# Kernel optimization log

Measured on AMD Instinct MI355X. Metric: run time of the kernel, lower is better.

## Reference

```python
import jax, jax.numpy as jnp
import numpy as np

HIDDEN = 128
N_RBF = 20
K = 16
CUTOFF = 5.0


def setup_inputs() -> dict:
    key = jax.random.key(0)
    ks = jax.random.split(key, 12)
    B, N, D = 8, 4096, HIDDEN
    edge_in = 2 * D + N_RBF  # 276
    s = 0.02
    return {
        "h": jax.random.normal(ks[0], (B, N, D), jnp.float32),
        "positions": jax.random.normal(ks[1], (B, N, 3), jnp.float32),
        # edge MLP: Linear(276->128), SiLU, Linear(128->128), SiLU
        "ew1": jax.random.normal(ks[2], (edge_in, D), jnp.float32) * s,
        "eb1": jnp.zeros((D,), jnp.float32),
        "ew2": jax.random.normal(ks[3], (D, D), jnp.float32) * s,
        "eb2": jnp.zeros((D,), jnp.float32),
        # node MLP: Linear(256->128), SiLU, (Dropout=identity in eval), Linear(128->128)
        "nw1": jax.random.normal(ks[4], (2 * D, D), jnp.float32) * s,
        "nb1": jnp.zeros((D,), jnp.float32),
        "nw2": jax.random.normal(ks[5], (D, D), jnp.float32) * s,
        "nb2": jnp.zeros((D,), jnp.float32),
        # LayerNorm
        "gamma": jnp.ones((D,), jnp.float32),
        "beta": jnp.zeros((D,), jnp.float32),
    }


def reference(h, positions, ew1, eb1, ew2, eb2, nw1, nb1, nw2, nb2, gamma, beta):
    B, N, D = h.shape
    k = min(K, N - 1)

    # ---- kNN graph build (dense pairwise, self masked with +inf) ----
    diff = positions[:, :, None, :] - positions[:, None, :, :]      # [B,N,N,3]
    dists = jnp.sqrt(jnp.sum(diff * diff, axis=-1) + 1e-8)          # [B,N,N]
    eye = jnp.eye(N, dtype=bool)
    dists_masked = jnp.where(eye[None], jnp.inf, dists)
    _, edge_idx = jax.lax.top_k(-dists_masked, k)                   # [B,N,k] smallest dists
    edge_dist = jnp.take_along_axis(dists_masked, edge_idx, axis=-1)  # [B,N,k]
    edge_mask = edge_dist < CUTOFF                                  # [B,N,k]

    # ---- RBF distance encoding (non-trainable buffers) ----
    centers = jnp.linspace(0.0, CUTOFF, N_RBF)                      # [n_rbf]
    widths = (CUTOFF / N_RBF) ** (-2)
    rbf = jnp.exp(-widths * (edge_dist[..., None] - centers) ** 2)  # [B,N,k,n_rbf]

    # ---- gather neighbor features ----
    h_j = jax.vmap(lambda hb, ib: hb[ib])(h, edge_idx)              # [B,N,k,D]
    h_i = jnp.broadcast_to(h[:, :, None, :], h_j.shape)             # [B,N,k,D]
    edge_features = jnp.concatenate([h_i, h_j, rbf], axis=-1)       # [B,N,k,2D+n_rbf]

    # ---- edge MLP + mask + scatter-sum aggregate ----
    m = jax.nn.silu(edge_features @ ew1 + eb1)
    m = jax.nn.silu(m @ ew2 + eb2)
    m = m * edge_mask[..., None].astype(m.dtype)
    agg = jnp.sum(m, axis=2)                                        # [B,N,D]

    # ---- node MLP (dropout is identity at eval) + residual + LayerNorm ----
    node_in = jnp.concatenate([h, agg], axis=-1)                    # [B,N,2D]
    update = jax.nn.silu(node_in @ nw1 + nb1) @ nw2 + nb2
    x = h + update
    mu = jnp.mean(x, axis=-1, keepdims=True)
    var = jnp.mean((x - mu) ** 2, axis=-1, keepdims=True)
    return (x - mu) / jnp.sqrt(var + 1e-5) * gamma + beta
```

## Files before the change

### kernel.cpp

```cpp
#include <hip/hip_runtime.h>

#define HID 128
#define NRBF 20
#define KNN 16
#define NNODE 4096
#define NBATCH 8
#define CAP 112

typedef __attribute__((ext_vector_type(8))) short short8;
typedef __attribute__((ext_vector_type(4))) float f32x4;

__device__ __forceinline__ short f2bf(float x) {
  unsigned u = __builtin_bit_cast(unsigned, x);
  u = u + 0x7FFFu + ((u >> 16) & 1u);
  return (short)(u >> 16);
}
__device__ __forceinline__ float silu_f(float x) {
  return x * __builtin_amdgcn_rcpf(1.0f + __expf(-x));
}
__device__ __forceinline__ short8 cv8(const float* p) {
  f32x4 a = *(const f32x4*)p;
  f32x4 b = *(const f32x4*)(p + 4);
  short8 r;
  r[0]=f2bf(a[0]); r[1]=f2bf(a[1]); r[2]=f2bf(a[2]); r[3]=f2bf(a[3]);
  r[4]=f2bf(b[0]); r[5]=f2bf(b[1]); r[6]=f2bf(b[2]); r[7]=f2bf(b[3]);
  return r;
}

__global__ __launch_bounds__(256)
void hcvt_kernel(const float* __restrict__ h, short* __restrict__ hb)
{
  size_t i = ((size_t)blockIdx.x * 256 + threadIdx.x) * 8;
  *(short8*)(hb + i) = cv8(h + i);
}

__global__ __launch_bounds__(512)
void knn_kernel(const float* __restrict__ pos,
                int* __restrict__ eidx, float* __restrict__ edist)
{
  __shared__ float pX[NNODE], pY[NNODE], pZ[NNODE];
  __shared__ float d2b[8][4][CAP];
  __shared__ int   jb[8][4][CAP];
  __shared__ int   cntL[8][4];

  const int tid  = threadIdx.x;
  const int wv   = tid >> 6;
  const int lane = tid & 63;
  const int b    = blockIdx.x >> 7;
  const int grp  = blockIdx.x & 127;

  const float* pb = pos + (size_t)b * NNODE * 3;
  for (int idx = tid; idx < NNODE; idx += 512) {
    pX[idx] = pb[idx*3]; pY[idx] = pb[idx*3+1]; pZ[idx] = pb[idx*3+2];
  }
  __syncthreads();

  const int i0 = grp * 32 + wv * 4;
  float pix[4], piy[4], piz[4];
  #pragma unroll
  for (int n = 0; n < 4; ++n) { pix[n]=pX[i0+n]; piy[n]=pY[i0+n]; piz[n]=pZ[i0+n]; }

  float vmin[4] = {3.0e38f, 3.0e38f, 3.0e38f, 3.0e38f};
  #pragma unroll 4
  for (int t = 0; t < 64; ++t) {
    const int j = t * 64 + lane;
    const float x = pX[j], y = pY[j], z = pZ[j];
    #pragma unroll
    for (int n = 0; n < 4; ++n) {
      float dx = __fsub_rn(pix[n], x);
      float dy = __fsub_rn(piy[n], y);
      float dz = __fsub_rn(piz[n], z);
      float d2 = __fadd_rn(__fadd_rn(__fmul_rn(dx,dx), __fmul_rn(dy,dy)), __fmul_rn(dz,dz));
      vmin[n] = fminf(vmin[n], d2);
    }
  }

  float Ts[4];
  #pragma unroll
  for (int n = 0; n < 4; ++n) {
    float v = vmin[n];
    #pragma unroll
    for (int k = 2; k <= 64; k <<= 1) {
      #pragma unroll
      for (int jj = k >> 1; jj > 0; jj >>= 1) {
        float o = __shfl_xor(v, jj);
        const bool up   = ((lane & k) == 0);
        const bool lowl = ((lane & jj) == 0);
        float mn = fminf(v, o), mx = fmaxf(v, o);
        v = (up == lowl) ? mn : mx;
      }
    }
    Ts[n] = __shfl(v, 16);
  }

  if (lane < 4) cntL[wv][lane] = 0;
  #pragma unroll 2
  for (int t = 0; t < 64; ++t) {
    const int j = t * 64 + lane;
    const float x = pX[j], y = pY[j], z = pZ[j];
    #pragma unroll
    for (int n = 0; n < 4; ++n) {
      float dx = __fsub_rn(pix[n], x);
      float dy = __fsub_rn(piy[n], y);
      float dz = __fsub_rn(piz[n], z);
      float d2 = __fadd_rn(__fadd_rn(__fmul_rn(dx,dx), __fmul_rn(dy,dy)), __fmul_rn(dz,dz));
      if ((j != i0 + n) && (d2 <= Ts[n])) {
        int p = atomicAdd(&cntL[wv][n], 1);
        if (p < CAP) { d2b[wv][n][p] = d2; jb[wv][n][p] = j; }
      }
    }
  }

  #pragma unroll 1
  for (int n = 0; n < 4; ++n) {
    int cnt = cntL[wv][n];
    if (cnt > CAP) cnt = CAP;
    for (int s = lane; s < cnt; s += 64) {
      float dm = d2b[wv][n][s]; int jm = jb[wv][n][s];
      int rank = 0;
      for (int c = 0; c < cnt; ++c) {
        float dc = d2b[wv][n][c]; int jc = jb[wv][n][c];
        if (dc < dm || (dc == dm && jc < jm)) ++rank;
      }
      if (rank < KNN) {
        size_t base = ((size_t)b * NNODE + i0 + n) * KNN;
        eidx[base + rank]  = b * NNODE + jm;
        edist[base + rank] = sqrtf(__fadd_rn(dm, 1e-8f));
      }
    }
  }
}

#define ENPW 16

template<bool HBF>
__global__ __launch_bounds__(512)
void edge_kernel(const float* __restrict__ h, const short* __restrict__ hb,
                 const int* __restrict__ eidx, const float* __restrict__ edist,
                 const float* __restrict__ ew1, const float* __restrict__ eb1,
                 const float* __restrict__ ew2, const float* __restrict__ eb2,
                 float* __restrict__ agg)
{
  __shared__ __attribute__((aligned(16))) short8 F1[9*8*64];
  __shared__ __attribute__((aligned(16))) short8 F2[4*8*64];
  __shared__ __attribute__((aligned(16))) short m1s[8][2048];

  const int tid = threadIdx.x;
  for (int f = tid; f < 9*8*64; f += 512) {
    int kc = f >> 9, rem = f & 511, nf = rem >> 6, ln = rem & 63;
    int kb = kc*32 + (ln >> 4)*8, col = nf*16 + (ln & 15);
    short8 v;
    #pragma unroll
    for (int e = 0; e < 8; ++e) {
      int k = kb + e;
      v[e] = (k < 276) ? f2bf(ew1[k*128 + col]) : (short)0;
    }
    F1[f] = v;
  }
  for (int f = tid; f < 4*8*64; f += 512) {
    int kc = f >> 9, rem = f & 511, nf = rem >> 6, ln = rem & 63;
    int kb = kc*32 + (ln >> 4)*8, col = nf*16 + (ln & 15);
    short8 v;
    #pragma unroll
    for (int e = 0; e < 8; ++e) v[e] = f2bf(ew2[(kb + e)*128 + col]);
    F2[f] = v;
  }
  __syncthreads();

  const int wv = tid >> 6, lane = tid & 63;
  const int lo = lane & 15, hi = lane >> 4;
  short* m1w = &m1s[wv][0];

  float b1v[8], b2v[8];
  #pragma unroll
  for (int nf = 0; nf < 8; ++nf) {
    b1v[nf] = eb1[nf*16 + lo];
    b2v[nf] = eb2[nf*16 + lo];
  }
  int wbase[4], xmask[4], rbase[4];
  #pragma unroll
  for (int q = 0; q < 4; ++q) {
    int row = hi*4 + q;
    wbase[q] = (row << 8) + (lo << 1);
    xmask[q] = (row & 7) << 4;
  }
  #pragma unroll
  for (int kc = 0; kc < 4; ++kc)
    rbase[kc] = ((lo << 8) + ((kc*32 + hi*8) << 1)) ^ ((lo & 7) << 4);

  const f32x4 zero4 = {0.f, 0.f, 0.f, 0.f};
  const int nbase = (blockIdx.x * 8 + wv) * ENPW;

  #pragma unroll 1
  for (int it = 0; it < ENPW/2; ++it) {
    const int nA = nbase + it*2, nB = nA + 1;
    int jgA = eidx[(size_t)nA*KNN + lo] & (NBATCH*NNODE - 1);
    int jgB = eidx[(size_t)nB*KNN + lo] & (NBATCH*NNODE - 1);
    const float deA = edist[(size_t)nA*KNN + lo];
    const float deB = edist[(size_t)nB*KNN + lo];

    short8 aIA[4], aJA[4], aIB[4], aJB[4];
    #pragma unroll
    for (int kc = 0; kc < 4; ++kc) {
      if constexpr (HBF) {
        aIA[kc] = *(const short8*)(hb + (size_t)nA*HID  + kc*32 + hi*8);
        aJA[kc] = *(const short8*)(hb + (size_t)jgA*HID + kc*32 + hi*8);
        aIB[kc] = *(const short8*)(hb + (size_t)nB*HID  + kc*32 + hi*8);
        aJB[kc] = *(const short8*)(hb + (size_t)jgB*HID + kc*32 + hi*8);
      } else {
        aIA[kc] = cv8(h + (size_t)nA*HID  + kc*32 + hi*8);
        aJA[kc] = cv8(h + (size_t)jgA*HID + kc*32 + hi*8);
        aIB[kc] = cv8(h + (size_t)nB*HID  + kc*32 + hi*8);
        aJB[kc] = cv8(h + (size_t)jgB*HID + kc*32 + hi*8);
      }
    }
    short8 aRA, aRB;
    #pragma unroll
    for (int e = 0; e < 8; ++e) {
      const int r = hi*8 + e;
      float vA = 0.f, vB = 0.f;
      if (r < NRBF) {
        const float cr = (float)(r * (5.0/19.0));
        float tA = __fsub_rn(deA, cr), tB = __fsub_rn(deB, cr);
        vA = __expf(-16.0f * __fmul_rn(tA, tA));
        vB = __expf(-16.0f * __fmul_rn(tB, tB));
      }
      aRA[e] = f2bf(vA); aRB[e] = f2bf(vB);
    }

    f32x4 acc1A[8], acc1B[8];
    #pragma unroll
    for (int nf = 0; nf < 8; ++nf) { acc1A[nf] = zero4; acc1B[nf] = zero4; }
    __builtin_amdgcn_s_setprio(1);
    #pragma unroll
    for (int kc = 0; kc < 9; ++kc) {
      short8 aA = (kc < 4) ? aIA[kc] : ((kc < 8) ? aJA[kc-4] : aRA);
      short8 aB = (kc < 4) ? aIB[kc] : ((kc < 8) ? aJB[kc-4] : aRB);
      #pragma unroll
      for (int nf = 0; nf < 8; ++nf) {
        short8 bf = F1[(kc*8 + nf)*64 + lane];
        acc1A[nf] = __builtin_amdgcn_mfma_f32_16x16x32_bf16(aA, bf, acc1A[nf], 0,0,0);
        acc1B[nf] = __builtin_amdgcn_mfma_f32_16x16x32_bf16(aB, bf, acc1B[nf], 0,0,0);
      }
    }
    __builtin_amdgcn_s_setprio(0);

    short8 a2A[4], a2B[4];
    #pragma unroll
    for (int nf = 0; nf < 8; ++nf) {
      #pragma unroll
      for (int q = 0; q < 4; ++q) {
        int off = (wbase[q] + (nf << 5)) ^ xmask[q];
        *(short*)((char*)m1w + off) = f2bf(silu_f(acc1A[nf][q] + b1v[nf]));
      }
    }
    #pragma unroll
    for (int kc = 0; kc < 4; ++kc)
      a2A[kc] = *(const short8*)((char*)m1w + rbase[kc]);
    #pragma unroll
    for (int nf = 0; nf < 8; ++nf) {
      #pragma unroll
      for (int q = 0; q < 4; ++q) {
        int off = (wbase[q] + (nf << 5)) ^ xmask[q];
        *(short*)((char*)m1w + off) = f2bf(silu_f(acc1B[nf][q] + b1v[nf]));
      }
    }
    #pragma unroll
    for (int kc = 0; kc < 4; ++kc)
      a2B[kc] = *(const short8*)((char*)m1w + rbase[kc]);

    f32x4 acc2A[8], acc2B[8];
    #pragma unroll
    for (int nf = 0; nf < 8; ++nf) { acc2A[nf] = zero4; acc2B[nf] = zero4; }
    __builtin_amdgcn_s_setprio(1);
    #pragma unroll
    for (int kc = 0; kc < 4; ++kc) {
      #pragma unroll
      for (int nf = 0; nf < 8; ++nf) {
        short8 bf = F2[(kc*8 + nf)*64 + lane];
        acc2A[nf] = __builtin_amdgcn_mfma_f32_16x16x32_bf16(a2A[kc], bf, acc2A[nf], 0,0,0);
        acc2B[nf] = __builtin_amdgcn_mfma_f32_16x16x32_bf16(a2B[kc], bf, acc2B[nf], 0,0,0);
      }
    }
    __builtin_amdgcn_s_setprio(0);

    float dqA[4], dqB[4];
    #pragma unroll
    for (int q = 0; q < 4; ++q) {
      dqA[q] = edist[(size_t)nA*KNN + hi*4 + q];
      dqB[q] = edist[(size_t)nB*KNN + hi*4 + q];
    }
    #pragma unroll
    for (int nf = 0; nf < 8; ++nf) {
      float sA = 0.f, sB = 0.f;
      #pragma unroll
      for (int q = 0; q < 4; ++q) {
        float mA = silu_f(acc2A[nf][q] + b2v[nf]);
        float mB = silu_f(acc2B[nf][q] + b2v[nf]);
        sA += (dqA[q] < 5.0f) ? mA : 0.f;
        sB += (dqB[q] < 5.0f) ? mB : 0.f;
      }
      sA += __shfl_xor(sA, 16); sA += __shfl_xor(sA, 32);
      sB += __shfl_xor(sB, 16); sB += __shfl_xor(sB, 32);
      if (hi == 0) {
        agg[(size_t)nA*HID + nf*16 + lo] = sA;
        agg[(size_t)nB*HID + nf*16 + lo] = sB;
      }
    }
  }
}

template<bool HBF>
__global__ __launch_bounds__(512)
void node_kernel(const float* __restrict__ h, const short* __restrict__ hb,
                 const float* agg,
                 const float* __restrict__ nw1, const float* __restrict__ nb1,
                 const float* __restrict__ nw2, const float* __restrict__ nb2,
                 const float* __restrict__ gam, const float* __restrict__ bet,
                 float* out)
{
  __shared__ __attribute__((aligned(16))) short8 G1[8*8*64];
  __shared__ __attribute__((aligned(16))) short8 G2[4*8*64];
  __shared__ __attribute__((aligned(16))) short m1s[8][2048];

  const int tid = threadIdx.x;
  for (int f = tid; f < 8*8*64; f += 512) {
    int kc = f >> 9, rem = f & 511, nf = rem >> 6, ln = rem & 63;
    int kb = kc*32 + (ln >> 4)*8, col = nf*16 + (ln & 15);
    short8 v;
    #pragma unroll
    for (int e = 0; e < 8; ++e) v[e] = f2bf(nw1[(kb + e)*128 + col]);
    G1[f] = v;
  }
  for (int f = tid; f < 4*8*64; f += 512) {
    int kc = f >> 9, rem = f & 511, nf = rem >> 6, ln = rem & 63;
    int kb = kc*32 + (ln >> 4)*8, col = nf*16 + (ln & 15);
    short8 v;
    #pragma unroll
    for (int e = 0; e < 8; ++e) v[e] = f2bf(nw2[(kb + e)*128 + col]);
    G2[f] = v;
  }
  __syncthreads();

  const int wv = tid >> 6, lane = tid & 63;
  const int lo = lane & 15, hi = lane >> 4;
  short* m1w = &m1s[wv][0];

  float b1v[8], b2v[8], gv[8], bv[8];
  #pragma unroll
  for (int nf = 0; nf < 8; ++nf) {
    b1v[nf] = nb1[nf*16 + lo];
    b2v[nf] = nb2[nf*16 + lo];
    gv[nf]  = gam[nf*16 + lo];
    bv[nf]  = bet[nf*16 + lo];
  }
  const f32x4 zero4 = {0.f, 0.f, 0.f, 0.f};

  const int row0 = (blockIdx.x * 8 + wv) * 16;

  const float* hrow = h   + (size_t)(row0 + lo) * HID;
  const float* arow = agg + (size_t)(row0 + lo) * HID;
  const short* hbrow = hb + (size_t)(row0 + lo) * HID;

  f32x4 acc1[8];
  #pragma unroll
  for (int nf = 0; nf < 8; ++nf) acc1[nf] = zero4;
  #pragma unroll
  for (int kc = 0; kc < 8; ++kc) {
    short8 a;
    if (kc < 4) {
      if constexpr (HBF) a = *(const short8*)(hbrow + kc*32 + hi*8);
      else               a = cv8(hrow + kc*32 + hi*8);
    } else {
      a = cv8(arow + (kc - 4)*32 + hi*8);
    }
    #pragma unroll
    for (int nf = 0; nf < 8; ++nf) {
      short8 bf = G1[(kc*8 + nf)*64 + lane];
      acc1[nf] = __builtin_amdgcn_mfma_f32_16x16x32_bf16(a, bf, acc1[nf], 0,0,0);
    }
  }

  #pragma unroll
  for (int nf = 0; nf < 8; ++nf) {
    #pragma unroll
    for (int q = 0; q < 4; ++q) {
      float s = silu_f(acc1[nf][q] + b1v[nf]);
      int row = hi*4 + q, col = nf*16 + lo;
      int byteoff = ((row << 8) + (col << 1)) ^ ((row & 7) << 4);
      *(short*)((char*)m1w + byteoff) = f2bf(s);
    }
  }

  f32x4 acc2[8];
  #pragma unroll
  for (int nf = 0; nf < 8; ++nf) acc2[nf] = zero4;
  #pragma unroll
  for (int kc = 0; kc < 4; ++kc) {
    int byteA = ((lo << 8) + ((kc*32 + hi*8) << 1)) ^ ((lo & 7) << 4);
    short8 a = *(const short8*)((char*)m1w + byteA);
    #pragma unroll
    for (int nf = 0; nf < 8; ++nf) {
      short8 bf = G2[(kc*8 + nf)*64 + lane];
      acc2[nf] = __builtin_amdgcn_mfma_f32_16x16x32_bf16(a, bf, acc2[nf], 0,0,0);
    }
  }

  float xv[4][8];
  #pragma unroll
  for (int nf = 0; nf < 8; ++nf) {
    #pragma unroll
    for (int q = 0; q < 4; ++q) {
      xv[q][nf] = acc2[nf][q] + b2v[nf]
                + h[(size_t)(row0 + hi*4 + q) * HID + nf*16 + lo];
    }
  }

  #pragma unroll
  for (int q = 0; q < 4; ++q) {
    float s = 0.0f;
    #pragma unroll
    for (int nf = 0; nf < 8; ++nf) s += xv[q][nf];
    s += __shfl_xor(s, 1); s += __shfl_xor(s, 2);
    s += __shfl_xor(s, 4); s += __shfl_xor(s, 8);
    float mu = s * 0.0078125f;
    float t = 0.0f;
    #pragma unroll
    for (int nf = 0; nf < 8; ++nf) { float d = xv[q][nf] - mu; t += d * d; }
    t += __shfl_xor(t, 1); t += __shfl_xor(t, 2);
    t += __shfl_xor(t, 4); t += __shfl_xor(t, 8);
    float inv = 1.0f / sqrtf(t * 0.0078125f + 1e-5f);
    #pragma unroll
    for (int nf = 0; nf < 8; ++nf) {
      float y = (xv[q][nf] - mu) * inv * gv[nf] + bv[nf];
      out[(size_t)(row0 + hi*4 + q) * HID + nf*16 + lo] = y;
    }
  }
}

extern "C" void kernel_launch(void* const* d_in, const int* in_sizes, int n_in,
                              void* d_out, int out_size, void* d_ws, size_t ws_size,
                              hipStream_t stream) {
  (void)in_sizes; (void)n_in; (void)out_size;
  const float* h   = (const float*)d_in[0];
  const float* pos = (const float*)d_in[1];
  const float* ew1 = (const float*)d_in[2];
  const float* eb1 = (const float*)d_in[3];
  const float* ew2 = (const float*)d_in[4];
  const float* eb2 = (const float*)d_in[5];
  const float* nw1 = (const float*)d_in[6];
  const float* nb1 = (const float*)d_in[7];
  const float* nw2 = (const float*)d_in[8];
  const float* nb2 = (const float*)d_in[9];
  const float* gam = (const float*)d_in[10];
  const float* bet = (const float*)d_in[11];

  const size_t base_need = (size_t)NBATCH * NNODE * KNN * 8;
  const size_t hbf_need  = base_need + (size_t)NBATCH * NNODE * HID * 2;
  if (ws_size < base_need) return;
  const bool use_hbf = (ws_size >= hbf_need);

  char* wsp = (char*)d_ws;
  int*   eidx  = (int*)wsp;
  float* edist = (float*)(wsp + (size_t)NBATCH * NNODE * KNN * 4);
  short* hb    = (short*)(wsp + base_need);
  float* agg   = (float*)d_out;

  if (use_hbf) {
    hcvt_kernel<<<dim3(2048), dim3(256), 0, stream>>>(h, hb);
  }
  knn_kernel<<<dim3(1024), dim3(512), 0, stream>>>(pos, eidx, edist);
  if (use_hbf) {
    edge_kernel<true ><<<dim3(256), dim3(512), 0, stream>>>(h, hb, eidx, edist,
                                                            ew1, eb1, ew2, eb2, agg);
    node_kernel<true ><<<dim3(256), dim3(512), 0, stream>>>(h, hb, agg, nw1, nb1,
                                                            nw2, nb2, gam, bet, (float*)d_out);
  } else {
    edge_kernel<false><<<dim3(256), dim3(512), 0, stream>>>(h, hb, eidx, edist,
                                                            ew1, eb1, ew2, eb2, agg);
    node_kernel<false><<<dim3(256), dim3(512), 0, stream>>>(h, hb, agg, nw1, nb1,
                                                            nw2, nb2, gam, bet, (float*)d_out);
  }
}
```

Measured before the change: 211.7 us.

## Double edge-kernel waves per block and halve per-wave LDS staging buffer

The edge kernel now launches 1024 threads (16 waves) per block, and each wave handles 8 nodes instead of 16. The per-wave LDS staging buffer for the first-layer activations is halved, so it is written and read in two half-width passes with a new XOR swizzle. The per-row distance mask values are now taken by cross-lane shuffle of already-loaded distances instead of reloading them from global memory. The aim is more waves in flight to hide gather latency. The 1024-thread launch bound squeezes the register budget, which risks spills given the large accumulator arrays.

```diff
diff --git a/kernel.cpp b/kernel.cpp
--- a/kernel.cpp
+++ b/kernel.cpp
@@ -131,10 +131,10 @@
   }
 }
 
-#define ENPW 16
+#define ENPW 8
 
 template<bool HBF>
-__global__ __launch_bounds__(512)
+__global__ __launch_bounds__(1024)
 void edge_kernel(const float* __restrict__ h, const short* __restrict__ hb,
                  const int* __restrict__ eidx, const float* __restrict__ edist,
                  const float* __restrict__ ew1, const float* __restrict__ eb1,
@@ -143,10 +143,10 @@
 {
   __shared__ __attribute__((aligned(16))) short8 F1[9*8*64];
   __shared__ __attribute__((aligned(16))) short8 F2[4*8*64];
-  __shared__ __attribute__((aligned(16))) short m1s[8][2048];
+  __shared__ __attribute__((aligned(16))) short m1s[16][1024];
 
   const int tid = threadIdx.x;
-  for (int f = tid; f < 9*8*64; f += 512) {
+  for (int f = tid; f < 9*8*64; f += 1024) {
     int kc = f >> 9, rem = f & 511, nf = rem >> 6, ln = rem & 63;
     int kb = kc*32 + (ln >> 4)*8, col = nf*16 + (ln & 15);
     short8 v;
@@ -157,7 +157,7 @@
     }
     F1[f] = v;
   }
-  for (int f = tid; f < 4*8*64; f += 512) {
+  for (int f = tid; f < 4*8*64; f += 1024) {
     int kc = f >> 9, rem = f & 511, nf = rem >> 6, ln = rem & 63;
     int kb = kc*32 + (ln >> 4)*8, col = nf*16 + (ln & 15);
     short8 v;
@@ -177,19 +177,21 @@
     b1v[nf] = eb1[nf*16 + lo];
     b2v[nf] = eb2[nf*16 + lo];
   }
-  int wbase[4], xmask[4], rbase[4];
+  int wrow[4], wkey[4], rb[2];
   #pragma unroll
   for (int q = 0; q < 4; ++q) {
     int row = hi*4 + q;
-    wbase[q] = (row << 8) + (lo << 1);
-    xmask[q] = (row & 7) << 4;
-  }
-  #pragma unroll
-  for (int kc = 0; kc < 4; ++kc)
-    rbase[kc] = ((lo << 8) + ((kc*32 + hi*8) << 1)) ^ ((lo & 7) << 4);
+    wrow[q] = row << 7;
+    wkey[q] = row & 7;
+  }
+  const int inb = (lo & 7) << 1;
+  const int slotb0 = (lo >> 3);
+  #pragma unroll
+  for (int kcl = 0; kcl < 2; ++kcl)
+    rb[kcl] = (lo << 7) + (((kcl*4 + hi) ^ (lo & 7)) << 4);
 
   const f32x4 zero4 = {0.f, 0.f, 0.f, 0.f};
-  const int nbase = (blockIdx.x * 8 + wv) * ENPW;
+  const int nbase = (blockIdx.x * 16 + wv) * ENPW;
 
   #pragma unroll 1
   for (int it = 0; it < ENPW/2; ++it) {
@@ -247,27 +249,39 @@
 
     short8 a2A[4], a2B[4];
     #pragma unroll
-    for (int nf = 0; nf < 8; ++nf) {
-      #pragma unroll
-      for (int q = 0; q < 4; ++q) {
-        int off = (wbase[q] + (nf << 5)) ^ xmask[q];
-        *(short*)((char*)m1w + off) = f2bf(silu_f(acc1A[nf][q] + b1v[nf]));
-      }
-    }
-    #pragma unroll
-    for (int kc = 0; kc < 4; ++kc)
-      a2A[kc] = *(const short8*)((char*)m1w + rbase[kc]);
-    #pragma unroll
-    for (int nf = 0; nf < 8; ++nf) {
-      #pragma unroll
-      for (int q = 0; q < 4; ++q) {
-        int off = (wbase[q] + (nf << 5)) ^ xmask[q];
-        *(short*)((char*)m1w + off) = f2bf(silu_f(acc1B[nf][q] + b1v[nf]));
-      }
-    }
-    #pragma unroll
-    for (int kc = 0; kc < 4; ++kc)
-      a2B[kc] = *(const short8*)((char*)m1w + rbase[kc]);
+    for (int hh = 0; hh < 2; ++hh) {
+      #pragma unroll
+      for (int nfl = 0; nfl < 4; ++nfl) {
+        int nf = hh*4 + nfl;
+        int slot = nfl*2 + slotb0;
+        #pragma unroll
+        for (int q = 0; q < 4; ++q) {
+          float s = silu_f(acc1A[nf][q] + b1v[nf]);
+          int off = wrow[q] + ((slot ^ wkey[q]) << 4) + inb;
+          *(short*)((char*)m1w + off) = f2bf(s);
+        }
+      }
+      #pragma unroll
+      for (int kcl = 0; kcl < 2; ++kcl)
+        a2A[hh*2 + kcl] = *(const short8*)((char*)m1w + rb[kcl]);
+    }
+    #pragma unroll
+    for (int hh = 0; hh < 2; ++hh) {
+      #pragma unroll
+      for (int nfl = 0; nfl < 4; ++nfl) {
+        int nf = hh*4 + nfl;
+        int slot = nfl*2 + slotb0;
+        #pragma unroll
+        for (int q = 0; q < 4; ++q) {
+          float s = silu_f(acc1B[nf][q] + b1v[nf]);
+          int off = wrow[q] + ((slot ^ wkey[q]) << 4) + inb;
+          *(short*)((char*)m1w + off) = f2bf(s);
+        }
+      }
+      #pragma unroll
+      for (int kcl = 0; kcl < 2; ++kcl)
+        a2B[hh*2 + kcl] = *(const short8*)((char*)m1w + rb[kcl]);
+    }
 
     f32x4 acc2A[8], acc2B[8];
     #pragma unroll
@@ -287,8 +301,8 @@
     float dqA[4], dqB[4];
     #pragma unroll
     for (int q = 0; q < 4; ++q) {
-      dqA[q] = edist[(size_t)nA*KNN + hi*4 + q];
-      dqB[q] = edist[(size_t)nB*KNN + hi*4 + q];
+      dqA[q] = __shfl(deA, hi*4 + q);
+      dqB[q] = __shfl(deB, hi*4 + q);
     }
     #pragma unroll
     for (int nf = 0; nf < 8; ++nf) {
@@ -471,13 +485,13 @@
   }
   knn_kernel<<<dim3(1024), dim3(512), 0, stream>>>(pos, eidx, edist);
   if (use_hbf) {
-    edge_kernel<true ><<<dim3(256), dim3(512), 0, stream>>>(h, hb, eidx, edist,
-                                                            ew1, eb1, ew2, eb2, agg);
+    edge_kernel<true ><<<dim3(256), dim3(1024), 0, stream>>>(h, hb, eidx, edist,
+                                                             ew1, eb1, ew2, eb2, agg);
     node_kernel<true ><<<dim3(256), dim3(512), 0, stream>>>(h, hb, agg, nw1, nb1,
                                                             nw2, nb2, gam, bet, (float*)d_out);
   } else {
-    edge_kernel<false><<<dim3(256), dim3(512), 0, stream>>>(h, hb, eidx, edist,
-                                                            ew1, eb1, ew2, eb2, agg);
+    edge_kernel<false><<<dim3(256), dim3(1024), 0, stream>>>(h, hb, eidx, edist,
+                                                             ew1, eb1, ew2, eb2, agg);
     node_kernel<false><<<dim3(256), dim3(512), 0, stream>>>(h, hb, agg, nw1, nb1,
                                                             nw2, nb2, gam, bet, (float*)d_out);
   }
```

New measurement: 251.4 us. 1.19x slower.
